# Kernel optimization log

Hardware: AMD Instinct MI355X
Metric: run time of the kernel (lower is better)

Reference implementation:

```python
import jax, jax.numpy as jnp
import numpy as np

NEG_SLOPE = 0.2
DIMS = [128, 32, 64, 128, 256]
NUM_GRAPHS = 64


def _glorot(key, shape):
    fan_in, fan_out = shape[0], shape[-1]
    lim = np.sqrt(6.0 / (fan_in + fan_out))
    return jax.random.uniform(key, shape, jnp.float32, -lim, lim)


def setup_inputs() -> dict:
    key = jax.random.key(0)
    ks = jax.random.split(key, 32)
    N, E = 100000, 1600000
    inp = {
        "x": jax.random.normal(ks[0], (N, DIMS[0]), jnp.float32),
        "edge_index": jax.random.randint(ks[1], (2, E), 0, N, jnp.int64),
        "batch": jnp.sort(jax.random.randint(ks[2], (N,), 0, NUM_GRAPHS, jnp.int64)),
    }
    ki = 3
    for l in range(4):
        din, dout = DIMS[l], DIMS[l + 1]
        inp[f"W{l+1}"] = _glorot(ks[ki], (din, dout)); ki += 1
        inp[f"a_src{l+1}"] = _glorot(ks[ki], (dout,)); ki += 1
        inp[f"a_dst{l+1}"] = _glorot(ks[ki], (dout,)); ki += 1
        inp[f"b{l+1}"] = jnp.zeros((dout,), jnp.float32)
    inp["lin1_w"] = _glorot(ks[ki], (256, 128)); ki += 1
    inp["lin1_b"] = jnp.zeros((128,), jnp.float32)
    inp["lin2_w"] = _glorot(ks[ki], (128, 10)); ki += 1
    inp["lin2_b"] = jnp.zeros((10,), jnp.float32)
    return inp


def _gat_layer(x, src, dst, W, a_src, a_dst, b, N):
    # PyG GATConv, heads=1: h = xW; e_ij = leaky_relu(a_src.h_j + a_dst.h_i)
    h = x @ W                                   # [N, dout]
    al_s = h @ a_src                            # [N]
    al_d = h @ a_dst                            # [N]
    e = jax.nn.leaky_relu(al_s[src] + al_d[dst], NEG_SLOPE)  # [E]
    # segment softmax over destination node neighborhoods
    e_max = jax.ops.segment_max(e, dst, num_segments=N)
    ex = jnp.exp(e - e_max[dst])
    denom = jax.ops.segment_sum(ex, dst, num_segments=N)
    alpha = ex / denom[dst]                     # [E]
    out = jax.ops.segment_sum(alpha[:, None] * h[src], dst, num_segments=N)
    return out + b


def reference(x, edge_index, batch,
              W1, a_src1, a_dst1, b1, W2, a_src2, a_dst2, b2,
              W3, a_src3, a_dst3, b3, W4, a_src4, a_dst4, b4,
              lin1_w, lin1_b, lin2_w, lin2_b):
    N = x.shape[0]
    # add self loops (PyG GATConv default)
    loop = jnp.arange(N, dtype=edge_index.dtype)
    src = jnp.concatenate([edge_index[0], loop])
    dst = jnp.concatenate([edge_index[1], loop])
    x = jax.nn.elu(_gat_layer(x, src, dst, W1, a_src1, a_dst1, b1, N))
    x = jax.nn.elu(_gat_layer(x, src, dst, W2, a_src2, a_dst2, b2, N))
    x = jax.nn.elu(_gat_layer(x, src, dst, W3, a_src3, a_dst3, b3, N))
    x = jax.nn.elu(_gat_layer(x, src, dst, W4, a_src4, a_dst4, b4, N))
    # global mean pool over graphs
    sums = jax.ops.segment_sum(x, batch, num_segments=NUM_GRAPHS)
    cnts = jax.ops.segment_sum(jnp.ones((N,), x.dtype), batch, num_segments=NUM_GRAPHS)
    g = sums / jnp.maximum(cnts, 1.0)[:, None]  # [64, 256]
    # dropout is identity in eval mode
    g = jax.nn.elu(g @ lin1_w + lin1_b)
    return g @ lin2_w + lin2_b                  # [64, 10]
```

## Files before the change

kernel.cpp:

```cpp
#include <hip/hip_runtime.h>
#include <math.h>

#define NG 64
#define SC_CHUNK 2048
#define FILL_P 4

typedef unsigned int uint;
typedef unsigned short ushort;

__device__ __forceinline__ float leaky(float x){ return x > 0.f ? x : 0.2f*x; }

__device__ __forceinline__ ushort f2bf(float f){
  uint u = __float_as_uint(f);
  uint r = (u + 0x7FFFu + ((u >> 16) & 1u)) >> 16;
  return (ushort)r;
}

__device__ __forceinline__ int lowbound(const int* __restrict__ a, int n, int v){
  int lo = 0, hi = n;
  while (lo < hi){ int mid = (lo + hi) >> 1; if (a[mid] < v) lo = mid + 1; else hi = mid; }
  return lo;
}

__global__ void k_zero_i32(int* __restrict__ p, int n){
  int i = blockIdx.x * 256 + threadIdx.x; if (i < n) p[i] = 0;
}
__global__ void k_zero_f32(float* __restrict__ p, int n){
  int i = blockIdx.x * 256 + threadIdx.x; if (i < n) p[i] = 0.f;
}

__global__ void k_count(const int* __restrict__ ei, int E, int N, int* __restrict__ cnt){
  int e = blockIdx.x * 256 + threadIdx.x;
  if (e >= E + N) return;
  int d = (e < E) ? __builtin_nontemporal_load(ei + E + e) : (e - E);
  atomicAdd(&cnt[d], 1);
}

__global__ __launch_bounds__(256) void k_bsum(const int* __restrict__ cnt, int N,
                                              int* __restrict__ bsum){
  int b = blockIdx.x, t = threadIdx.x;
  int lo = b * SC_CHUNK, hi = min(lo + SC_CHUNK, N);
  int s = 0;
  for (int i = lo + t; i < hi; i += 256) s += cnt[i];
  for (int o = 32; o > 0; o >>= 1) s += __shfl_xor(s, o);
  __shared__ int ws[4];
  if ((t & 63) == 0) ws[t >> 6] = s;
  __syncthreads();
  if (t == 0) bsum[b] = ws[0] + ws[1] + ws[2] + ws[3];
}

__global__ __launch_bounds__(1024) void k_bscan(const int* __restrict__ bsum, int B,
                                                int* __restrict__ boff, int* __restrict__ total){
  __shared__ int sp[1024];
  int t = threadIdx.x;
  int v = (t < B) ? bsum[t] : 0;
  sp[t] = v;
  __syncthreads();
  for (int off = 1; off < 1024; off <<= 1){
    int u = (t >= off) ? sp[t - off] : 0;
    __syncthreads();
    sp[t] += u;
    __syncthreads();
  }
  if (t < B) boff[t] = sp[t] - v;
  if (t == 0) total[0] = (B > 0) ? sp[B - 1] : 0;
}

__global__ __launch_bounds__(256) void k_scatter(const int* __restrict__ cnt, int N,
                                                 const int* __restrict__ boff,
                                                 int* __restrict__ row_start, int* __restrict__ cur){
  int b = blockIdx.x, t = threadIdx.x;
  int base = b * SC_CHUNK + t * 8;
  int v[8]; int s = 0;
#pragma unroll
  for (int k = 0; k < 8; ++k){ int i = base + k; v[k] = (i < N) ? cnt[i] : 0; s += v[k]; }
  __shared__ int sp[256];
  sp[t] = s;
  __syncthreads();
  for (int off = 1; off < 256; off <<= 1){
    int u = (t >= off) ? sp[t - off] : 0;
    __syncthreads();
    sp[t] += u;
    __syncthreads();
  }
  int run = boff[b] + (t ? sp[t - 1] : 0);
#pragma unroll
  for (int k = 0; k < 8; ++k){
    int i = base + k;
    if (i < N){ row_start[i] = run; cur[i] = run; run += v[k]; }
  }
}

__global__ void k_fill(const int* __restrict__ ei, int E, int N, int dlo, int dhi,
                       int* __restrict__ cur, int* __restrict__ col){
  int e = blockIdx.x * 256 + threadIdx.x;
  if (e >= E + N) return;
  int s, d;
  if (e < E){
    d = __builtin_nontemporal_load(ei + E + e);
    s = __builtin_nontemporal_load(ei + e);
  } else { s = e - E; d = s; }
  if (d < dlo || d >= dhi) return;
  int pos = atomicAdd(&cur[d], 1);
  col[pos] = s;
}

template<int DIN, int DOUT, int BN>
__global__ __launch_bounds__(256) void k_gemm(const float* __restrict__ X,
                                              const float* __restrict__ W,
                                              ushort* __restrict__ H, int N){
  constexpr int BM = 128, BK = 32, TM = 8;
  constexpr int TN = BN / 16;
  static_assert(DIN % BK == 0 && DOUT % BN == 0 && (TN == 2 || TN == 4), "shape");
  __shared__ float xs[BK][BM];
  __shared__ float wsm[BK][BN];
  int m0 = blockIdx.x * BM;
  int n0 = blockIdx.y * BN;
  int tid = threadIdx.x;
  int tc = tid & 15, tr = tid >> 4;
  float acc[TM][TN];
#pragma unroll
  for (int i = 0; i < TM; ++i)
#pragma unroll
    for (int j = 0; j < TN; ++j) acc[i][j] = 0.f;

  for (int kt = 0; kt < DIN; kt += BK){
    __syncthreads();
    for (int t = tid; t < BM * BK / 4; t += 256){
      int m = t >> 3, kq = t & 7;
      float4 v = make_float4(0.f, 0.f, 0.f, 0.f);
      int row = m0 + m;
      if (row < N) v = *(const float4*)(X + (size_t)row * DIN + kt + kq * 4);
      xs[kq * 4 + 0][m] = v.x; xs[kq * 4 + 1][m] = v.y;
      xs[kq * 4 + 2][m] = v.z; xs[kq * 4 + 3][m] = v.w;
    }
    for (int t = tid; t < BK * BN / 4; t += 256){
      int k = t / (BN / 4), nq = t % (BN / 4);
      float4 v = *(const float4*)(W + (size_t)(kt + k) * DOUT + n0 + nq * 4);
      *(float4*)(&wsm[k][nq * 4]) = v;
    }
    __syncthreads();
#pragma unroll
    for (int k = 0; k < BK; ++k){
      float a[TM], b[TN];
      *(float4*)&a[0] = *(const float4*)&xs[k][tr * TM];
      *(float4*)&a[4] = *(const float4*)&xs[k][tr * TM + 4];
      if constexpr (TN == 4) *(float4*)&b[0] = *(const float4*)&wsm[k][tc * 4];
      else                   *(float2*)&b[0] = *(const float2*)&wsm[k][tc * 2];
#pragma unroll
      for (int i = 0; i < TM; ++i)
#pragma unroll
        for (int j = 0; j < TN; ++j) acc[i][j] = fmaf(a[i], b[j], acc[i][j]);
    }
  }
#pragma unroll
  for (int i = 0; i < TM; ++i){
    int row = m0 + tr * TM + i;
    if (row < N){
      if constexpr (TN == 4){
        uint2 pk;
        pk.x = (uint)f2bf(acc[i][0]) | ((uint)f2bf(acc[i][1]) << 16);
        pk.y = (uint)f2bf(acc[i][2]) | ((uint)f2bf(acc[i][3]) << 16);
        *(uint2*)&H[(size_t)row * DOUT + n0 + tc * 4] = pk;
      } else {
        uint pk = (uint)f2bf(acc[i][0]) | ((uint)f2bf(acc[i][1]) << 16);
        *(uint*)&H[(size_t)row * DOUT + n0 + tc * 2] = pk;
      }
    }
  }
}

template<int DOUT>
__global__ __launch_bounds__(256) void k_alpha(const ushort* __restrict__ H,
                                               const float* __restrict__ a_src,
                                               const float* __restrict__ a_dst,
                                               float* __restrict__ als, float* __restrict__ ald, int N){
  int wave = threadIdx.x >> 6, lane = threadIdx.x & 63;
  int i = blockIdx.x * 4 + wave;
  if (i >= N) return;
  constexpr int P = DOUT / 2;
  float ss = 0.f, sd = 0.f;
#pragma unroll
  for (int cb = 0; cb < (P + 63) / 64; ++cb){
    int p = cb * 64 + lane;
    if (P % 64 == 0 || p < P){
      uint u = ((const uint*)(H + (size_t)i * DOUT))[p];
      float f0 = __uint_as_float(u << 16);
      float f1 = __uint_as_float(u & 0xffff0000u);
      ss = fmaf(f0, a_src[2 * p], fmaf(f1, a_src[2 * p + 1], ss));
      sd = fmaf(f0, a_dst[2 * p], fmaf(f1, a_dst[2 * p + 1], sd));
    }
  }
  for (int o = 32; o > 0; o >>= 1){ ss += __shfl_xor(ss, o); sd += __shfl_xor(sd, o); }
  if (lane == 0){ als[i] = ss; ald[i] = sd; }
}

template<int VC>
__device__ __forceinline__ void gacc(float* a, const ushort* __restrict__ H, int DOUTv,
                                     int sn, float w, int cl){
  if constexpr (VC == 4){
    uint2 u = ((const uint2*)(H + (size_t)sn * DOUTv))[cl];
    a[0] = fmaf(w, __uint_as_float(u.x << 16),         a[0]);
    a[1] = fmaf(w, __uint_as_float(u.x & 0xffff0000u), a[1]);
    a[2] = fmaf(w, __uint_as_float(u.y << 16),         a[2]);
    a[3] = fmaf(w, __uint_as_float(u.y & 0xffff0000u), a[3]);
  } else {
    uint u = ((const uint*)(H + (size_t)sn * DOUTv))[cl];
    a[0] = fmaf(w, __uint_as_float(u << 16),           a[0]);
    a[1] = fmaf(w, __uint_as_float(u & 0xffff0000u),   a[1]);
  }
}

template<int DOUT>
__global__ __launch_bounds__(256) void k_agg3(const ushort* __restrict__ H,
                                              const int* __restrict__ rs,
                                              const int* __restrict__ col,
                                              const float* __restrict__ als,
                                              const float* __restrict__ ald,
                                              const float* __restrict__ bias,
                                              float* __restrict__ OUTB, int N){
  constexpr int VC = (DOUT >= 256) ? 4 : 2;
  constexpr int CL = (DOUT / VC > 64) ? 64 : DOUT / VC;
  constexpr int ES = 64 / CL;
  int wave = threadIdx.x >> 6, lane = threadIdx.x & 63;
  int i = blockIdx.x * 4 + wave;
  if (i >= N) return;
  int beg = rs[i], end = rs[i + 1], deg = end - beg;
  float ad = ald[i];
  int cl = lane & (CL - 1);

  float s = 0.f;
  float a0[VC], a1[VC], a2[VC], a3[VC];
#pragma unroll
  for (int c = 0; c < VC; ++c){ a0[c] = a1[c] = a2[c] = a3[c] = 0.f; }

  for (int base = 0; base < deg; base += 64){
    int off = base + lane;
    bool valid = off < deg;
    int   sn_v = valid ? col[beg + off] : 0;
    float w_v  = valid ? __expf(leaky(als[sn_v] + ad)) : 0.f;
    s += w_v;
    int cnt = min(64, deg - base);
    if constexpr (ES == 1){
      int k = 0;
      for (; k + 3 < cnt; k += 4){
        int   s0 = __shfl(sn_v, k),     s1 = __shfl(sn_v, k + 1);
        int   s2 = __shfl(sn_v, k + 2), s3 = __shfl(sn_v, k + 3);
        float w0 = __shfl(w_v, k),      w1 = __shfl(w_v, k + 1);
        float w2 = __shfl(w_v, k + 2),  w3 = __shfl(w_v, k + 3);
        gacc<VC>(a0, H, DOUT, s0, w0, cl);
        gacc<VC>(a1, H, DOUT, s1, w1, cl);
        gacc<VC>(a2, H, DOUT, s2, w2, cl);
        gacc<VC>(a3, H, DOUT, s3, w3, cl);
      }
      for (; k < cnt; ++k)
        gacc<VC>(a0, H, DOUT, __shfl(sn_v, k), __shfl(w_v, k), cl);
    } else {
      int es = lane >> (CL == 32 ? 5 : 4);
      int k = 0;
      for (; k + 2 * ES - 1 < cnt; k += 2 * ES){
        int e0 = k + es, e1 = k + ES + es;
        gacc<VC>(a0, H, DOUT, __shfl(sn_v, e0), __shfl(w_v, e0), cl);
        gacc<VC>(a1, H, DOUT, __shfl(sn_v, e1), __shfl(w_v, e1), cl);
      }
      for (; k < cnt; k += ES){
        int e0 = k + es;
        if (e0 < cnt)
          gacc<VC>(a0, H, DOUT, __shfl(sn_v, e0), __shfl(w_v, e0), cl);
      }
    }
  }
  for (int o = 32; o > 0; o >>= 1) s += __shfl_xor(s, o);
#pragma unroll
  for (int c = 0; c < VC; ++c) a0[c] = (a0[c] + a1[c]) + (a2[c] + a3[c]);
  if constexpr (ES > 1){
#pragma unroll
    for (int o = CL; o < 64; o <<= 1)
#pragma unroll
      for (int c = 0; c < VC; ++c) a0[c] += __shfl_xor(a0[c], o);
  }
  if (lane < CL){
    float inv = 1.0f / s;
    int ch = cl * VC;
    float o[VC];
#pragma unroll
    for (int c = 0; c < VC; ++c){
      float x = a0[c] * inv + bias[ch + c];
      o[c] = x > 0.f ? x : __expf(x) - 1.f;
    }
    if constexpr (VC == 4)
      *(float4*)&OUTB[(size_t)i * DOUT + ch] = make_float4(o[0], o[1], o[2], o[3]);
    else
      *(float2*)&OUTB[(size_t)i * DOUT + ch] = make_float2(o[0], o[1]);
  }
}

__global__ __launch_bounds__(256) void k_pool(const float* __restrict__ X4,
                                              const int* __restrict__ batch, int N,
                                              float* __restrict__ g){
  int ch = threadIdx.x;
  int nPer = (N + gridDim.x - 1) / gridDim.x;
  int n0 = blockIdx.x * nPer, n1 = min(n0 + nPer, N);
  if (n0 >= n1) return;
  float acc = 0.f;
  int cg = batch[n0];
  for (int n = n0; n < n1; ++n){
    int gb = batch[n];
    if (gb != cg){ atomicAdd(&g[cg * 256 + ch], acc); acc = 0.f; cg = gb; }
    acc += X4[(size_t)n * 256 + ch];
  }
  atomicAdd(&g[cg * 256 + ch], acc);
}

__global__ __launch_bounds__(128) void k_mlp(const float* __restrict__ g,
                                             const int* __restrict__ batch, int N,
                                             const float* __restrict__ l1w, const float* __restrict__ l1b,
                                             const float* __restrict__ l2w, const float* __restrict__ l2b,
                                             float* __restrict__ out){
  __shared__ float gb[256];
  __shared__ float hb[128];
  int gi = blockIdx.x, t = threadIdx.x;
  int lo = lowbound(batch, N, gi);
  int hi = lowbound(batch, N, gi + 1);
  float invc = 1.0f / fmaxf((float)(hi - lo), 1.0f);
  gb[t]       = g[gi * 256 + t] * invc;
  gb[t + 128] = g[gi * 256 + t + 128] * invc;
  __syncthreads();
  float s = l1b[t];
  for (int k = 0; k < 256; ++k) s = fmaf(gb[k], l1w[k * 128 + t], s);
  s = s > 0.f ? s : __expf(s) - 1.f;
  hb[t] = s;
  __syncthreads();
  if (t < 10){
    float o = l2b[t];
    for (int k = 0; k < 128; ++k) o = fmaf(hb[k], l2w[k * 10 + t], o);
    out[gi * 10 + t] = o;
  }
}

template<int DIN, int DOUT>
static void run_layer(const float* xin, const float* W, const float* asrc, const float* adst,
                      const float* bias, ushort* H, float* OUTB,
                      const int* rs, const int* col, float* als, float* ald,
                      int N, hipStream_t stream){
  constexpr int BN = (DOUT < 64) ? DOUT : 64;
  dim3 grid((N + 127) / 128, DOUT / BN);
  k_gemm<DIN, DOUT, BN><<<grid, 256, 0, stream>>>(xin, W, H, N);
  int nb = (N + 3) / 4;
  k_alpha<DOUT><<<nb, 256, 0, stream>>>(H, asrc, adst, als, ald, N);
  k_agg3<DOUT><<<nb, 256, 0, stream>>>(H, rs, col, als, ald, bias, OUTB, N);
}

extern "C" void kernel_launch(void* const* d_in, const int* in_sizes, int n_in,
                              void* d_out, int out_size, void* d_ws, size_t ws_size,
                              hipStream_t stream){
  const float* x     = (const float*)d_in[0];
  const int*   ei    = (const int*)  d_in[1];
  const int*   batch = (const int*)  d_in[2];
  const float* W1  = (const float*)d_in[3];
  const float* as1 = (const float*)d_in[4];
  const float* ad1 = (const float*)d_in[5];
  const float* b1  = (const float*)d_in[6];
  const float* W2  = (const float*)d_in[7];
  const float* as2 = (const float*)d_in[8];
  const float* ad2 = (const float*)d_in[9];
  const float* b2  = (const float*)d_in[10];
  const float* W3  = (const float*)d_in[11];
  const float* as3 = (const float*)d_in[12];
  const float* ad3 = (const float*)d_in[13];
  const float* b3  = (const float*)d_in[14];
  const float* W4  = (const float*)d_in[15];
  const float* as4 = (const float*)d_in[16];
  const float* ad4 = (const float*)d_in[17];
  const float* b4  = (const float*)d_in[18];
  const float* l1w = (const float*)d_in[19];
  const float* l1b = (const float*)d_in[20];
  const float* l2w = (const float*)d_in[21];
  const float* l2b = (const float*)d_in[22];

  int N  = in_sizes[2];
  int E  = in_sizes[1] / 2;
  int EN = E + N;
  int B  = (N + SC_CHUNK - 1) / SC_CHUNK;

  char* p = (char*)d_ws;
  auto alloc = [&](size_t bytes){ void* r = (void*)p; p += (bytes + 255) & ~(size_t)255; return r; };
  ushort* H    = (ushort*)alloc((size_t)N * 256 * 2);
  float*  OUTB = (float*) alloc((size_t)N * 256 * 4);
  int*    cnt  = (int*)   alloc((size_t)N * 4);
  int*    cur  = (int*)   alloc((size_t)N * 4);
  int*    rs   = (int*)   alloc((size_t)(N + 1) * 4);
  int*    col  = (int*)   alloc((size_t)EN * 4);
  float*  als  = (float*) alloc((size_t)N * 4);
  float*  ald  = (float*) alloc((size_t)N * 4);
  float*  g    = (float*) alloc((size_t)NG * 256 * 4);
  int*    bsum = (int*)   alloc((size_t)1024 * 4);
  int*    boff = (int*)   alloc((size_t)1024 * 4);

  k_zero_i32<<<(N + 255) / 256, 256, 0, stream>>>(cnt, N);
  k_count<<<(EN + 255) / 256, 256, 0, stream>>>(ei, E, N, cnt);
  k_bsum<<<B, 256, 0, stream>>>(cnt, N, bsum);
  k_bscan<<<1, 1024, 0, stream>>>(bsum, B, boff, rs + N);
  k_scatter<<<B, 256, 0, stream>>>(cnt, N, boff, rs, cur);
  {
    int W = (N + FILL_P - 1) / FILL_P;
    for (int pss = 0; pss < FILL_P; ++pss){
      int dlo = pss * W, dhi = min(dlo + W, N);
      if (dlo < dhi)
        k_fill<<<(EN + 255) / 256, 256, 0, stream>>>(ei, E, N, dlo, dhi, cur, col);
    }
  }

  run_layer<128,  32>(x,    W1, as1, ad1, b1, H, OUTB, rs, col, als, ald, N, stream);
  run_layer< 32,  64>(OUTB, W2, as2, ad2, b2, H, OUTB, rs, col, als, ald, N, stream);
  run_layer< 64, 128>(OUTB, W3, as3, ad3, b3, H, OUTB, rs, col, als, ald, N, stream);
  run_layer<128, 256>(OUTB, W4, as4, ad4, b4, H, OUTB, rs, col, als, ald, N, stream);

  k_zero_f32<<<(NG * 256 + 255) / 256, 256, 0, stream>>>(g, NG * 256);
  k_pool<<<1024, 256, 0, stream>>>(OUTB, batch, N, g);
  k_mlp<<<NG, 128, 0, stream>>>(g, batch, N, l1w, l1b, l2w, l2b, (float*)d_out);
}
```

Baseline: 782.9 us.

## Split wide-layer aggregation across channel halves with half-wave gathers

For layers with 128 or 256 output channels, aggregation now runs as a 2D grid where each block handles half the channels. Within each wave only 32 lanes gather bf16 features, while all 64 lanes compute edge weights and the four accumulator sets are kept as before. This is meant to raise parallelism and cut per-wave register and work load on the two widest layers, at the cost of recomputing edge weights and reloading col once per channel half. The fill kernel also checks the destination range before loading the source index, which skips a load for edges outside the range.

```diff
diff --git a/kernel.cpp b/kernel.cpp
--- a/kernel.cpp
+++ b/kernel.cpp
@@ -98,9 +98,12 @@
   int s, d;
   if (e < E){
     d = __builtin_nontemporal_load(ei + E + e);
+    if (d < dlo || d >= dhi) return;
     s = __builtin_nontemporal_load(ei + e);
-  } else { s = e - E; d = s; }
-  if (d < dlo || d >= dhi) return;
+  } else {
+    s = e - E; d = s;
+    if (d < dlo || d >= dhi) return;
+  }
   int pos = atomicAdd(&cur[d], 1);
   col[pos] = s;
 }
@@ -295,6 +298,74 @@
   }
 }
 
+template<int VC, int DOUT>
+__global__ __launch_bounds__(256) void k_aggS(const ushort* __restrict__ H,
+                                              const int* __restrict__ rs,
+                                              const int* __restrict__ col,
+                                              const float* __restrict__ als,
+                                              const float* __restrict__ ald,
+                                              const float* __restrict__ bias,
+                                              float* __restrict__ OUTB, int N){
+  int wave = threadIdx.x >> 6, lane = threadIdx.x & 63;
+  int i = blockIdx.x * 4 + wave;
+  if (i >= N) return;
+  int ch0 = blockIdx.y * (32 * VC);
+  const ushort* __restrict__ Tb = H + ch0;
+  int beg = rs[i], end = rs[i + 1], deg = end - beg;
+  float ad = ald[i];
+  int cl = lane & 31;
+  bool act = lane < 32;
+
+  float s = 0.f;
+  float a0[VC], a1[VC], a2[VC], a3[VC];
+#pragma unroll
+  for (int c = 0; c < VC; ++c){ a0[c] = a1[c] = a2[c] = a3[c] = 0.f; }
+
+  for (int base = 0; base < deg; base += 64){
+    int off = base + lane;
+    bool valid = off < deg;
+    int   sn_v = valid ? col[beg + off] : 0;
+    float w_v  = valid ? __expf(leaky(als[sn_v] + ad)) : 0.f;
+    s += w_v;
+    int cnt = min(64, deg - base);
+    int k = 0;
+    for (; k + 3 < cnt; k += 4){
+      int   s0 = __shfl(sn_v, k),     s1 = __shfl(sn_v, k + 1);
+      int   s2 = __shfl(sn_v, k + 2), s3 = __shfl(sn_v, k + 3);
+      float w0 = __shfl(w_v, k),      w1 = __shfl(w_v, k + 1);
+      float w2 = __shfl(w_v, k + 2),  w3 = __shfl(w_v, k + 3);
+      if (act){
+        gacc<VC>(a0, Tb, DOUT, s0, w0, cl);
+        gacc<VC>(a1, Tb, DOUT, s1, w1, cl);
+        gacc<VC>(a2, Tb, DOUT, s2, w2, cl);
+        gacc<VC>(a3, Tb, DOUT, s3, w3, cl);
+      }
+    }
+    for (; k < cnt; ++k){
+      int s0 = __shfl(sn_v, k); float w0 = __shfl(w_v, k);
+      if (act) gacc<VC>(a0, Tb, DOUT, s0, w0, cl);
+    }
+  }
+  for (int o = 32; o > 0; o >>= 1) s += __shfl_xor(s, o);
+#pragma unroll
+  for (int c = 0; c < VC; ++c) a0[c] = (a0[c] + a1[c]) + (a2[c] + a3[c]);
+
+  if (act){
+    float inv = 1.0f / s;
+    int ch = ch0 + cl * VC;
+    float o[VC];
+#pragma unroll
+    for (int c = 0; c < VC; ++c){
+      float x = a0[c] * inv + bias[ch + c];
+      o[c] = x > 0.f ? x : __expf(x) - 1.f;
+    }
+    if constexpr (VC == 4)
+      *(float4*)&OUTB[(size_t)i * DOUT + ch] = make_float4(o[0], o[1], o[2], o[3]);
+    else
+      *(float2*)&OUTB[(size_t)i * DOUT + ch] = make_float2(o[0], o[1]);
+  }
+}
+
 __global__ __launch_bounds__(256) void k_pool(const float* __restrict__ X4,
                                               const int* __restrict__ batch, int N,
                                               float* __restrict__ g){
@@ -348,7 +419,12 @@
   k_gemm<DIN, DOUT, BN><<<grid, 256, 0, stream>>>(xin, W, H, N);
   int nb = (N + 3) / 4;
   k_alpha<DOUT><<<nb, 256, 0, stream>>>(H, asrc, adst, als, ald, N);
-  k_agg3<DOUT><<<nb, 256, 0, stream>>>(H, rs, col, als, ald, bias, OUTB, N);
+  if constexpr (DOUT >= 128){
+    constexpr int VC = (DOUT >= 256) ? 4 : 2;
+    k_aggS<VC, DOUT><<<dim3(nb, 2), 256, 0, stream>>>(H, rs, col, als, ald, bias, OUTB, N);
+  } else {
+    k_agg3<DOUT><<<nb, 256, 0, stream>>>(H, rs, col, als, ald, bias, OUTB, N);
+  }
 }
 
 extern "C" void kernel_launch(void* const* d_in, const int* in_sizes, int n_in,
```

Result: slower. 915.8 us (+17.0%).
